# Kernel optimization log

Measured on AMD Instinct MI355X. Metric: run time of the kernel, lower is better.

Reference implementation:

```python
import jax, jax.numpy as jnp
import numpy as np

B, N, D_OBJ, D_Q, D_FUSED, D_BOX, D_ATT = 64, 36, 2048, 2048, 2048, 4, 512


def setup_inputs() -> dict:
    key = jax.random.key(0)
    ks = jax.random.split(key, 12)
    s = lambda d: 1.0 / np.sqrt(d)
    return {
        "question_embedding": jax.random.normal(ks[0], (B * N, D_Q), jnp.float32),
        "object_features_list": jax.random.normal(ks[1], (B, N, D_OBJ), jnp.float32),
        "bounding_boxes": jax.random.uniform(ks[2], (B, N, D_BOX), jnp.float32),
        "Wq": jax.random.normal(ks[3], (D_Q, D_FUSED), jnp.float32) * s(D_Q),
        "Wo": jax.random.normal(ks[4], (D_OBJ, D_FUSED), jnp.float32) * s(D_OBJ),
        "Wfa": jax.random.normal(ks[5], (D_FUSED, D_FUSED), jnp.float32) * s(D_FUSED),
        "Wfb": jax.random.normal(ks[6], (D_FUSED, D_FUSED), jnp.float32) * s(D_FUSED),
        "Wba": jax.random.normal(ks[7], (D_BOX, D_FUSED), jnp.float32) * s(D_BOX),
        "Wbb": jax.random.normal(ks[8], (D_BOX, D_FUSED), jnp.float32) * s(D_BOX),
        "W0": jax.random.normal(ks[9], (D_FUSED, D_ATT), jnp.float32) * s(D_FUSED),
        "b0": jnp.zeros((D_ATT,), jnp.float32),
        "W1": jax.random.normal(ks[10], (D_ATT, 1), jnp.float32) * s(D_ATT),
        "b1": jnp.zeros((1,), jnp.float32),
        "batch_size": B,
        "num_obj": N,
    }


def reference(question_embedding, object_features_list, bounding_boxes,
              Wq, Wo, Wfa, Wfb, Wba, Wbb, W0, b0, W1, b1,
              batch_size, num_obj):
    # fuse_object_features_with_questions: MLB fusion of question and objects
    obj_flat = object_features_list.reshape(batch_size * num_obj, -1)  # [BN, D]
    fused = (question_embedding @ Wq) * (obj_flat @ Wo)                # [BN, Df]
    fused = fused.reshape(batch_size, num_obj, -1)                     # [B, N, Df]

    # pairwise: project once, broadcast-multiply instead of materializing
    # expanded [B*N*N, D] operands (same math as expand+view+fusion).
    ra = fused @ Wfa                 # [B, N, Df]
    rb = fused @ Wfb                 # [B, N, Df]
    ba = bounding_boxes @ Wba        # [B, N, Df]
    bb = bounding_boxes @ Wbb        # [B, N, Df]
    # relations[b, i, j, :] = fusion_fused(f_i, f_j) + fusion_box(box_i, box_j)
    relations = ra[:, :, None, :] * rb[:, None, :, :] + ba[:, :, None, :] * bb[:, None, :, :]  # [B,N,N,Df]

    # compute_relation_attention: linear-tanh-linear, softmax over dim=2
    h = jnp.tanh(relations @ W0 + b0)          # [B, N, N, D_att]
    scores = h @ W1 + b1                       # [B, N, N, 1]
    att = jax.nn.softmax(scores, axis=2)[..., 0]  # [B, N, N]
    e_hat = jnp.sum(relations * att[..., None], axis=2)  # [B, N, Df]

    pairwise_res = fused + e_hat
    return object_features_list + pairwise_res
```

## Files before the change

### kernel.cpp

```cpp
#include <hip/hip_runtime.h>
#include <hip/hip_bf16.h>
#include <math.h>

constexpr int kB    = 64;
constexpr int kN    = 36;
constexpr int kBN   = kB * kN;
constexpr int kD    = 2048;
constexpr int kDatt = 512;
constexpr int kPairs = kN * kN;

using bf16x8 = __attribute__((ext_vector_type(8))) short;
using f32x4  = __attribute__((ext_vector_type(4))) float;

typedef unsigned int u32;
typedef __attribute__((address_space(3))) u32 lds_u32;
typedef const __attribute__((address_space(1))) u32 glb_u32;

__device__ inline unsigned short f2bf(float f) {
    union { float f; unsigned u; } v; v.f = f;
    unsigned r = v.u + 0x7FFFu + ((v.u >> 16) & 1u);
    return (unsigned short)(r >> 16);
}

__global__ __launch_bounds__(256)
void kcvt(const float* __restrict__ x, unsigned short* __restrict__ y, int n4)
{
    int i = blockIdx.x * 256 + threadIdx.x;
    if (i < n4) {
        float4 v = ((const float4*)x)[i];
        ushort4 o = {f2bf(v.x), f2bf(v.y), f2bf(v.z), f2bf(v.w)};
        ((ushort4*)y)[i] = o;
    }
}

__global__ __launch_bounds__(256)
void ktrp(const float* __restrict__ W, unsigned short* __restrict__ WT, int nt)
{
    __shared__ float T[64][65];
    const int k0 = blockIdx.x * 64;
    const int n0 = blockIdx.y * 64;
    const int c = threadIdx.x & 63, r0 = threadIdx.x >> 6;
    #pragma unroll
    for (int rr = 0; rr < 64; rr += 4)
        T[r0 + rr][c] = W[(size_t)(k0 + r0 + rr) * nt + n0 + c];
    __syncthreads();
    #pragma unroll
    for (int rr = 0; rr < 64; rr += 4)
        WT[(size_t)(n0 + r0 + rr) * kD + k0 + c] = f2bf(T[c][r0 + rr]);
}

__global__ __launch_bounds__(64)
void krepack_w0(const unsigned short* __restrict__ W0T, unsigned short* __restrict__ W0s)
{
    const int kb    = blockIdx.x;
    const int chunk = blockIdx.y;
    const int g     = threadIdx.x;
    const int row = chunk * 16 + (g & 7) + ((g >> 5) << 3);
    const int cg8 = ((g >> 3) & 3) * 8;
    const uint4 v = *(const uint4*)&W0T[(size_t)row * kD + kb * 32 + cg8];
    *(uint4*)&W0s[(size_t)kb * 16384 + chunk * 512 + g * 8] = v;
}

__global__ __launch_bounds__(128)
void kgbox(const float* __restrict__ Wba, const float* __restrict__ Wbb,
           const float* __restrict__ W0, float* __restrict__ G)
{
    const int uv = blockIdx.x;
    const int u = uv >> 2, v = uv & 3;
    const int c = blockIdx.y * 128 + threadIdx.x;
    float acc = 0.f;
    for (int k = 0; k < kD; k += 4) {
        #pragma unroll
        for (int t = 0; t < 4; ++t)
            acc = fmaf(Wba[u * kD + k + t] * Wbb[v * kD + k + t],
                       W0[(size_t)(k + t) * kDatt + c], acc);
    }
    G[(size_t)uv * kDatt + c] = acc;
}

__global__ __launch_bounds__(64)
void krepack_g(const float* __restrict__ G, unsigned short* __restrict__ W0s)
{
    const int chunk = blockIdx.x;
    const int g     = threadIdx.x;
    const int col = chunk * 16 + (g & 7) + ((g >> 5) << 3);
    const int kg  = (g >> 3) & 3;
    unsigned short o[8];
    #pragma unroll
    for (int e = 0; e < 8; ++e) {
        int kl = kg * 8 + e;
        o[e] = (kl < 16) ? f2bf(G[(size_t)kl * kDatt + col]) : (unsigned short)0;
    }
    *(uint4*)&W0s[(size_t)64 * 16384 + chunk * 512 + g * 8] = *(uint4*)o;
}

__global__ __launch_bounds__(256)
void k3_box_proj(const float* __restrict__ box, const float* __restrict__ Wba,
                 const float* __restrict__ Wbb,
                 float* __restrict__ ba, float* __restrict__ bb)
{
    const int r = blockIdx.y;
    const int c = blockIdx.x * 256 + threadIdx.x;
    const float x0 = box[r * 4 + 0], x1 = box[r * 4 + 1];
    const float x2 = box[r * 4 + 2], x3 = box[r * 4 + 3];
    float va = x0 * Wba[c] + x1 * Wba[kD + c] + x2 * Wba[2 * kD + c] + x3 * Wba[3 * kD + c];
    float vb = x0 * Wbb[c] + x1 * Wbb[kD + c] + x2 * Wbb[2 * kD + c] + x3 * Wbb[3 * kD + c];
    ba[(size_t)r * kD + c] = va;
    bb[(size_t)r * kD + c] = vb;
}

__device__ inline void stage128(const unsigned short* __restrict__ g,
                                int grow0, int k0,
                                unsigned short* lds, int w, int lane)
{
    const int sr = lane >> 2, sc = (lane & 3) * 8;
    #pragma unroll
    for (int t = 0; t < 2; ++t) {
        int r = w * 32 + t * 16;
        const unsigned short* gp = g + (size_t)(grow0 + r + sr) * kD + k0 + sc;
        __builtin_amdgcn_global_load_lds((glb_u32*)gp, (lds_u32*)(lds + r * 32), 16, 0, 0);
    }
}
__device__ inline void stage64(const unsigned short* __restrict__ g,
                               int grow0, int k0,
                               unsigned short* lds, int w, int lane)
{
    const int sr = lane >> 2, sc = (lane & 3) * 8;
    int r = w * 16;
    const unsigned short* gp = g + (size_t)(grow0 + r + sr) * kD + k0 + sc;
    __builtin_amdgcn_global_load_lds((glb_u32*)gp, (lds_u32*)(lds + r * 32), 16, 0, 0);
}

__global__ __launch_bounds__(256, 2)
void k1_dual_mfma(const unsigned short* __restrict__ Qb,
                  const unsigned short* __restrict__ WqT,
                  const unsigned short* __restrict__ Ob,
                  const unsigned short* __restrict__ WoT,
                  unsigned short* __restrict__ fusedb)
{
    __shared__ __align__(16) unsigned short As1[128][32];
    __shared__ __align__(16) unsigned short As2[128][32];
    __shared__ __align__(16) unsigned short Bs1[64][32];
    __shared__ __align__(16) unsigned short Bs2[64][32];

    const int tid = threadIdx.x;
    const int lane = tid & 63;
    const int w = tid >> 6;
    const int wm = w >> 1, wn = w & 1;
    const int row0 = blockIdx.y * 128;
    const int col0 = blockIdx.x * 64;

    f32x4 acc1[4][2], acc2[4][2];
    #pragma unroll
    for (int mt = 0; mt < 4; ++mt)
        #pragma unroll
        for (int nt = 0; nt < 2; ++nt) { acc1[mt][nt] = (f32x4)(0.f); acc2[mt][nt] = (f32x4)(0.f); }

    const int fr = lane & 15, ko = (lane >> 4) * 8;

    for (int k0 = 0; k0 < kD; k0 += 32) {
        stage128(Qb,  row0, k0, &As1[0][0], w, lane);
        stage128(Ob,  row0, k0, &As2[0][0], w, lane);
        stage64 (WqT, col0, k0, &Bs1[0][0], w, lane);
        stage64 (WoT, col0, k0, &Bs2[0][0], w, lane);
        __syncthreads();

        bf16x8 a1[4], a2[4];
        #pragma unroll
        for (int mt = 0; mt < 4; ++mt) {
            a1[mt] = *(bf16x8*)&As1[wm * 64 + mt * 16 + fr][ko];
            a2[mt] = *(bf16x8*)&As2[wm * 64 + mt * 16 + fr][ko];
        }
        #pragma unroll
        for (int nt = 0; nt < 2; ++nt) {
            bf16x8 b1 = *(bf16x8*)&Bs1[wn * 32 + nt * 16 + fr][ko];
            bf16x8 b2 = *(bf16x8*)&Bs2[wn * 32 + nt * 16 + fr][ko];
            #pragma unroll
            for (int mt = 0; mt < 4; ++mt) {
                acc1[mt][nt] = __builtin_amdgcn_mfma_f32_16x16x32_bf16(a1[mt], b1, acc1[mt][nt], 0, 0, 0);
                acc2[mt][nt] = __builtin_amdgcn_mfma_f32_16x16x32_bf16(a2[mt], b2, acc2[mt][nt], 0, 0, 0);
            }
        }
        __syncthreads();
    }

    const int fq = lane >> 4;
    #pragma unroll
    for (int mt = 0; mt < 4; ++mt)
        #pragma unroll
        for (int nt = 0; nt < 2; ++nt) {
            int row = row0 + wm * 64 + mt * 16 + fq * 4;
            int col = col0 + wn * 32 + nt * 16 + fr;
            #pragma unroll
            for (int reg = 0; reg < 4; ++reg) {
                float v = acc1[mt][nt][reg] * acc2[mt][nt][reg];
                fusedb[(size_t)(row + reg) * kD + col] = f2bf(v);
            }
        }
}

__global__ __launch_bounds__(256, 2)
void k2_dual_mfma(const unsigned short* __restrict__ Fb,
                  const unsigned short* __restrict__ WfaT,
                  const unsigned short* __restrict__ WfbT,
                  float* __restrict__ ra, float* __restrict__ rb)
{
    __shared__ __align__(16) unsigned short As [128][32];
    __shared__ __align__(16) unsigned short Bs1[64][32];
    __shared__ __align__(16) unsigned short Bs2[64][32];

    const int tid = threadIdx.x;
    const int lane = tid & 63;
    const int w = tid >> 6;
    const int wm = w >> 1, wn = w & 1;
    const int row0 = blockIdx.y * 128;
    const int col0 = blockIdx.x * 64;

    f32x4 acc1[4][2], acc2[4][2];
    #pragma unroll
    for (int mt = 0; mt < 4; ++mt)
        #pragma unroll
        for (int nt = 0; nt < 2; ++nt) { acc1[mt][nt] = (f32x4)(0.f); acc2[mt][nt] = (f32x4)(0.f); }

    const int fr = lane & 15, ko = (lane >> 4) * 8;

    for (int k0 = 0; k0 < kD; k0 += 32) {
        stage128(Fb,   row0, k0, &As [0][0], w, lane);
        stage64 (WfaT, col0, k0, &Bs1[0][0], w, lane);
        stage64 (WfbT, col0, k0, &Bs2[0][0], w, lane);
        __syncthreads();

        bf16x8 a[4];
        #pragma unroll
        for (int mt = 0; mt < 4; ++mt)
            a[mt] = *(bf16x8*)&As[wm * 64 + mt * 16 + fr][ko];
        #pragma unroll
        for (int nt = 0; nt < 2; ++nt) {
            bf16x8 b1 = *(bf16x8*)&Bs1[wn * 32 + nt * 16 + fr][ko];
            bf16x8 b2 = *(bf16x8*)&Bs2[wn * 32 + nt * 16 + fr][ko];
            #pragma unroll
            for (int mt = 0; mt < 4; ++mt) {
                acc1[mt][nt] = __builtin_amdgcn_mfma_f32_16x16x32_bf16(a[mt], b1, acc1[mt][nt], 0, 0, 0);
                acc2[mt][nt] = __builtin_amdgcn_mfma_f32_16x16x32_bf16(a[mt], b2, acc2[mt][nt], 0, 0, 0);
            }
        }
        __syncthreads();
    }

    const int fq = lane >> 4;
    #pragma unroll
    for (int mt = 0; mt < 4; ++mt)
        #pragma unroll
        for (int nt = 0; nt < 2; ++nt) {
            int row = row0 + wm * 64 + mt * 16 + fq * 4;
            int col = col0 + wn * 32 + nt * 16 + fr;
            #pragma unroll
            for (int reg = 0; reg < 4; ++reg) {
                size_t o = (size_t)(row + reg) * kD + col;
                ra[o] = acc1[mt][nt][reg];
                rb[o] = acc2[mt][nt][reg];
            }
        }
}

__global__ __launch_bounds__(1024)
void k4_scores_mfma(const float* __restrict__ ra, const float* __restrict__ rb,
                    const float* __restrict__ box,
                    const unsigned short* __restrict__ W0s,
                    const float* __restrict__ b0, const float* __restrict__ W1,
                    float* __restrict__ scores)
{
    __shared__ __align__(16) unsigned short Bs[2][512 * 32];
    __shared__ __align__(16) unsigned short RelS[2][128][40];
    __shared__ __align__(16) float4 Stg4[2][378];
    __shared__ float scoreS[128];

    const int tid  = threadIdx.x;
    const int lane = tid & 63;
    const int w    = tid >> 6;
    const int wm   = w >> 3;
    const int wn   = w & 7;

    const int work = (blockIdx.x & 7) * 88 + (blockIdx.x >> 3);
    const int b    = work / 11;
    const int tile = work - b * 11;
    const int p0   = tile * 128;
    const int i0   = p0 / kN;

    const float* raB  = ra  + (size_t)b * kN * kD;
    const float* rbB  = rb  + (size_t)b * kN * kD;
    const float* boxB = box + (size_t)b * kN * 4;

    const bool hasStage = (tid < 336);
    const float* sptr;
    int sdst;
    {
        int s = hasStage ? tid : 335;
        int row = s >> 3, q = s & 7;
        int grow; const float* base;
        if (row < 6) {
            int il = (row < 5) ? row : 4;
            grow = i0 + il; if (grow > kN - 1) grow = kN - 1;
            base = raB;
        } else {
            grow = row - 6;
            base = rbB;
        }
        sptr = base + (size_t)grow * kD + q * 4;
        sdst = row * 9 + q;
    }

    int rowA, cgA, ilA, iA, jA;
    {
        rowA = tid >> 3; cgA = tid & 7;
        int p = p0 + rowA; if (p >= kPairs) p = kPairs - 1;
        iA  = p / kN;
        jA  = p - iA * kN;
        ilA = iA - i0;
    }

    const int fr = lane & 15, fq = lane >> 4;
    const int bco = ((fr & 7) << 3) + ((fr >> 3) << 8) + (fq << 6);

    f32x4 acc[4][4];
    #pragma unroll
    for (int mt = 0; mt < 4; ++mt)
        #pragma unroll
        for (int nt = 0; nt < 4; ++nt)
            acc[mt][nt] = (f32x4)(0.f);

    if (tid < 128) scoreS[tid] = 0.f;

    float4 sreg0;

    #define ISSUE_B(k0_, buf_)                                                   \
        _Pragma("unroll")                                                        \
        for (int t = 0; t < 2; ++t) {                                            \
            int chunk = w * 2 + t;                                               \
            const unsigned short* gp = W0s + (size_t)((k0_) >> 5) * 16384        \
                                       + chunk * 512 + lane * 8;                 \
            __builtin_amdgcn_global_load_lds((glb_u32*)gp,                       \
                (lds_u32*)&Bs[buf_][chunk * 512], 16, 0, 0);                     \
        }

    #define STAGE_LOAD(k0_) {                                                    \
            if (hasStage) sreg0 = *(const float4*)(sptr + (k0_));                \
        }

    #define STAGE_WRITE(buf_) {                                                  \
            if (hasStage) Stg4[buf_][sdst] = sreg0;                              \
        }

    #define REL_GEN(buf_) {                                                      \
            float4 va = Stg4[buf_][ilA * 9 + cgA];                               \
            float4 vr = Stg4[buf_][(6 + jA) * 9 + cgA];                          \
            ushort4 o;                                                           \
            o.x = f2bf(va.x * vr.x);                                             \
            o.y = f2bf(va.y * vr.y);                                             \
            o.z = f2bf(va.z * vr.z);                                             \
            o.w = f2bf(va.w * vr.w);                                             \
            *(ushort4*)&RelS[buf_][rowA][cgA * 4] = o;                           \
        }

    #define REL_GEN_BOX(buf_) {                                                  \
            ushort4 o = {0, 0, 0, 0};                                            \
            if (cgA < 4) {                                                       \
                float4 bi = *(const float4*)(boxB + iA * 4);                     \
                float4 bj = *(const float4*)(boxB + jA * 4);                     \
                float biu = (cgA == 0) ? bi.x : (cgA == 1) ? bi.y                \
                          : (cgA == 2) ? bi.z : bi.w;                            \
                o.x = f2bf(biu * bj.x);                                          \
                o.y = f2bf(biu * bj.y);                                          \
                o.z = f2bf(biu * bj.z);                                          \
                o.w = f2bf(biu * bj.w);                                          \
            }                                                                    \
            *(ushort4*)&RelS[buf_][rowA][cgA * 4] = o;                           \
        }

    STAGE_LOAD(0)
    STAGE_WRITE(0)
    STAGE_LOAD(32)
    __syncthreads();
    REL_GEN(0)
    STAGE_WRITE(1)
    ISSUE_B(0, 0)

    for (int k = 0; k <= 64; ++k) {
        const int cur = k & 1, nxt = cur ^ 1;
        __syncthreads();
        if (k < 62) STAGE_LOAD((k + 2) * 32)
        if (k < 64) ISSUE_B((k + 1) * 32, nxt)
        bf16x8 af[4];
        #pragma unroll
        for (int mt = 0; mt < 4; ++mt)
            af[mt] = *(bf16x8*)&RelS[cur][wm * 64 + mt * 16 + fr][fq * 8];
        #pragma unroll
        for (int nt = 0; nt < 4; ++nt) {
            bf16x8 bfv = *(bf16x8*)&Bs[cur][wn * 2048 + nt * 512 + bco];
            #pragma unroll
            for (int mt = 0; mt < 4; ++mt)
                acc[mt][nt] = __builtin_amdgcn_mfma_f32_16x16x32_bf16(af[mt], bfv, acc[mt][nt], 0, 0, 0);
        }
        if (k < 62) STAGE_WRITE(cur)
        if (k < 63) REL_GEN(nxt)
        else if (k == 63) REL_GEN_BOX(nxt)
    }

    float b0v[4], w1v[4];
    #pragma unroll
    for (int nt = 0; nt < 4; ++nt) {
        int col = wn * 64 + nt * 16 + fr;
        b0v[nt] = b0[col];
        w1v[nt] = W1[col];
    }
    #pragma unroll
    for (int mt = 0; mt < 4; ++mt) {
        #pragma unroll
        for (int reg = 0; reg < 4; ++reg) {
            float p = 0.f;
            #pragma unroll
            for (int nt = 0; nt < 4; ++nt)
                p += w1v[nt] * tanhf(acc[mt][nt][reg] + b0v[nt]);
            p += __shfl_xor(p, 1, 64);
            p += __shfl_xor(p, 2, 64);
            p += __shfl_xor(p, 4, 64);
            p += __shfl_xor(p, 8, 64);
            if (fr == 0)
                atomicAdd(&scoreS[wm * 64 + mt * 16 + fq * 4 + reg], p);
        }
    }
    __syncthreads();
    if (tid < 128 && p0 + tid < kPairs)
        scores[(size_t)b * kPairs + p0 + tid] = scoreS[tid];
}

__global__ __launch_bounds__(64)
void k5_softmax(const float* __restrict__ scores, float* __restrict__ att)
{
    const int bi = blockIdx.x;
    const int tid = threadIdx.x;
    float s = (tid < kN) ? scores[(size_t)bi * kN + tid] : -1e30f;
    float m = s;
    #pragma unroll
    for (int off = 32; off >= 1; off >>= 1)
        m = fmaxf(m, __shfl_xor(m, off, 64));
    float e = (tid < kN) ? expf(s - m) : 0.f;
    float sum = e;
    #pragma unroll
    for (int off = 32; off >= 1; off >>= 1)
        sum += __shfl_xor(sum, off, 64);
    if (tid < kN) att[(size_t)bi * kN + tid] = e / sum;
}

__global__ __launch_bounds__(256)
void k6_output(const float* __restrict__ obj, const unsigned short* __restrict__ fusedb,
               const float* __restrict__ ra, const float* __restrict__ ba,
               const float* __restrict__ rb, const float* __restrict__ bb,
               const float* __restrict__ att, float* __restrict__ out)
{
    __shared__ float attS[kN];
    const int bi = blockIdx.x;
    const int b = bi / kN;
    const int tid = threadIdx.x;
    if (tid < kN) attS[tid] = att[(size_t)bi * kN + tid];
    __syncthreads();
    for (int d = tid; d < kD; d += 256) {
        float s1 = 0.f, s2 = 0.f;
        #pragma unroll 4
        for (int j = 0; j < kN; ++j) {
            float a = attS[j];
            size_t rrow = (size_t)(b * kN + j) * kD + d;
            s1 = fmaf(a, rb[rrow], s1);
            s2 = fmaf(a, bb[rrow], s2);
        }
        size_t o = (size_t)bi * kD + d;
        float fv = __uint_as_float((u32)fusedb[o] << 16);
        out[o] = obj[o] + fv + ra[o] * s1 + ba[o] * s2;
    }
}

extern "C" void kernel_launch(void* const* d_in, const int* in_sizes, int n_in,
                              void* d_out, int out_size, void* d_ws, size_t ws_size,
                              hipStream_t stream)
{
    const float* q   = (const float*)d_in[0];
    const float* obj = (const float*)d_in[1];
    const float* box = (const float*)d_in[2];
    const float* Wq  = (const float*)d_in[3];
    const float* Wo  = (const float*)d_in[4];
    const float* Wfa = (const float*)d_in[5];
    const float* Wfb = (const float*)d_in[6];
    const float* Wba = (const float*)d_in[7];
    const float* Wbb = (const float*)d_in[8];
    const float* W0  = (const float*)d_in[9];
    const float* b0v = (const float*)d_in[10];
    const float* W1  = (const float*)d_in[11];
    float* out = (float*)d_out;

    const size_t nBD = (size_t)kBN * kD;
    float* ws = (float*)d_ws;
    size_t off = 0;
    float* ra     = ws + off; off += nBD;
    float* rb     = ws + off; off += nBD;
    float* ba     = ws + off; off += nBD;
    float* bb     = ws + off; off += nBD;
    float* scores = ws + off; off += (size_t)kBN * kN;
    float* att    = ws + off; off += (size_t)kBN * kN;
    float* G      = ws + off; off += (size_t)16 * kDatt;

    unsigned short* us = (unsigned short*)(ws + off);
    size_t uoff = 0;
    unsigned short* W0T     = us + uoff; uoff += (size_t)kDatt * kD;
    unsigned short* W0s     = us + uoff; uoff += (size_t)65 * 16384;
    unsigned short* q_bf    = us + uoff; uoff += nBD;
    unsigned short* obj_bf  = us + uoff; uoff += nBD;
    unsigned short* fusedbf = us + uoff; uoff += nBD;
    unsigned short* WqT     = us + uoff; uoff += (size_t)kD * kD;
    unsigned short* WoT     = us + uoff; uoff += (size_t)kD * kD;
    unsigned short* WfaT = q_bf;
    unsigned short* WfbT = obj_bf;

    const int n4 = (int)(nBD / 4);
    kcvt<<<dim3((n4 + 255) / 256), 256, 0, stream>>>(q,   q_bf,   n4);
    kcvt<<<dim3((n4 + 255) / 256), 256, 0, stream>>>(obj, obj_bf, n4);
    ktrp<<<dim3(32, 32), 256, 0, stream>>>(Wq, WqT, kD);
    ktrp<<<dim3(32, 32), 256, 0, stream>>>(Wo, WoT, kD);
    ktrp<<<dim3(32, 8),  256, 0, stream>>>(W0, W0T, kDatt);
    krepack_w0<<<dim3(kD / 32, kDatt / 16), 64, 0, stream>>>(W0T, W0s);
    kgbox<<<dim3(16, 4), 128, 0, stream>>>(Wba, Wbb, W0, G);
    krepack_g<<<dim3(32), 64, 0, stream>>>(G, W0s);
    k3_box_proj<<<dim3(kD / 256, kBN), 256, 0, stream>>>(box, Wba, Wbb, ba, bb);

    k1_dual_mfma<<<dim3(kD / 64, kBN / 128), 256, 0, stream>>>(q_bf, WqT, obj_bf, WoT, fusedbf);

    ktrp<<<dim3(32, 32), 256, 0, stream>>>(Wfa, WfaT, kD);
    ktrp<<<dim3(32, 32), 256, 0, stream>>>(Wfb, WfbT, kD);

    k2_dual_mfma<<<dim3(kD / 64, kBN / 128), 256, 0, stream>>>(fusedbf, WfaT, WfbT, ra, rb);

    k4_scores_mfma<<<dim3(kB * 11), 1024, 0, stream>>>(ra, rb, box, W0s, b0v, W1, scores);
    k5_softmax<<<kBN, 64, 0, stream>>>(scores, att);
    k6_output<<<kBN, 256, 0, stream>>>(obj, fusedbf, ra, ba, rb, bb, att, out);
}
```

Measured before the change: 760.9 us.

## Eliminate ba/bb materialization via attention-weighted boxes and split-K kgbox

Removes the k3_box_proj kernel and the two full [BN,2048] fp32 ba/bb buffers. The softmax kernel now also computes the attention-weighted box sum per row, and the output kernel rebuilds ba and the weighted bb sum on the fly from the 4-wide box projections, so bb is never streamed per j. kgbox is also restructured as a split-K kernel computing all 16 box-pair products per thread, with partial sums reduced in krepack_g, to use more parallelism than the old 64-block grid. This saves large memory writes and reads at the cost of a few extra FMAs and small weight loads in the output kernel.

```diff
diff --git a/kernel.cpp b/kernel.cpp
--- a/kernel.cpp
+++ b/kernel.cpp
@@ -61,25 +61,51 @@
     *(uint4*)&W0s[(size_t)kb * 16384 + chunk * 512 + g * 8] = v;
 }
 
-__global__ __launch_bounds__(128)
+__global__ __launch_bounds__(256)
 void kgbox(const float* __restrict__ Wba, const float* __restrict__ Wbb,
-           const float* __restrict__ W0, float* __restrict__ G)
-{
-    const int uv = blockIdx.x;
-    const int u = uv >> 2, v = uv & 3;
-    const int c = blockIdx.y * 128 + threadIdx.x;
-    float acc = 0.f;
-    for (int k = 0; k < kD; k += 4) {
-        #pragma unroll
-        for (int t = 0; t < 4; ++t)
-            acc = fmaf(Wba[u * kD + k + t] * Wbb[v * kD + k + t],
-                       W0[(size_t)(k + t) * kDatt + c], acc);
-    }
-    G[(size_t)uv * kDatt + c] = acc;
+           const float* __restrict__ W0, float* __restrict__ Gpart)
+{
+    __shared__ float red[4][64][17];
+    const int ct = blockIdx.x;
+    const int kc = blockIdx.y;
+    const int cl = threadIdx.x & 63;
+    const int kq = threadIdx.x >> 6;
+    const int c  = ct * 64 + cl;
+
+    float acc[16];
+    #pragma unroll
+    for (int t = 0; t < 16; ++t) acc[t] = 0.f;
+
+    const int kbase = kc * 128 + kq * 32;
+    for (int kk = 0; kk < 32; ++kk) {
+        int k = kbase + kk;
+        float w0 = W0[(size_t)k * kDatt + c];
+        float a0 = Wba[k], a1 = Wba[kD + k], a2 = Wba[2 * kD + k], a3 = Wba[3 * kD + k];
+        float b0 = Wbb[k] * w0, b1 = Wbb[kD + k] * w0,
+              b2 = Wbb[2 * kD + k] * w0, b3 = Wbb[3 * kD + k] * w0;
+        acc[0]  = fmaf(a0, b0, acc[0]);  acc[1]  = fmaf(a0, b1, acc[1]);
+        acc[2]  = fmaf(a0, b2, acc[2]);  acc[3]  = fmaf(a0, b3, acc[3]);
+        acc[4]  = fmaf(a1, b0, acc[4]);  acc[5]  = fmaf(a1, b1, acc[5]);
+        acc[6]  = fmaf(a1, b2, acc[6]);  acc[7]  = fmaf(a1, b3, acc[7]);
+        acc[8]  = fmaf(a2, b0, acc[8]);  acc[9]  = fmaf(a2, b1, acc[9]);
+        acc[10] = fmaf(a2, b2, acc[10]); acc[11] = fmaf(a2, b3, acc[11]);
+        acc[12] = fmaf(a3, b0, acc[12]); acc[13] = fmaf(a3, b1, acc[13]);
+        acc[14] = fmaf(a3, b2, acc[14]); acc[15] = fmaf(a3, b3, acc[15]);
+    }
+    #pragma unroll
+    for (int t = 0; t < 16; ++t) red[kq][cl][t] = acc[t];
+    __syncthreads();
+    #pragma unroll
+    for (int t = 0; t < 4; ++t) {
+        int s = threadIdx.x + t * 256;
+        int cc = s >> 4, uv = s & 15;
+        float v = red[0][cc][uv] + red[1][cc][uv] + red[2][cc][uv] + red[3][cc][uv];
+        Gpart[((size_t)kc * 16 + uv) * kDatt + ct * 64 + cc] = v;
+    }
 }
 
 __global__ __launch_bounds__(64)
-void krepack_g(const float* __restrict__ G, unsigned short* __restrict__ W0s)
+void krepack_g(const float* __restrict__ Gpart, unsigned short* __restrict__ W0s)
 {
     const int chunk = blockIdx.x;
     const int g     = threadIdx.x;
@@ -89,24 +115,15 @@
     #pragma unroll
     for (int e = 0; e < 8; ++e) {
         int kl = kg * 8 + e;
-        o[e] = (kl < 16) ? f2bf(G[(size_t)kl * kDatt + col]) : (unsigned short)0;
+        if (kl < 16) {
+            float s = 0.f;
+            #pragma unroll
+            for (int kc = 0; kc < 16; ++kc)
+                s += Gpart[((size_t)kc * 16 + kl) * kDatt + col];
+            o[e] = f2bf(s);
+        } else o[e] = 0;
     }
     *(uint4*)&W0s[(size_t)64 * 16384 + chunk * 512 + g * 8] = *(uint4*)o;
-}
-
-__global__ __launch_bounds__(256)
-void k3_box_proj(const float* __restrict__ box, const float* __restrict__ Wba,
-                 const float* __restrict__ Wbb,
-                 float* __restrict__ ba, float* __restrict__ bb)
-{
-    const int r = blockIdx.y;
-    const int c = blockIdx.x * 256 + threadIdx.x;
-    const float x0 = box[r * 4 + 0], x1 = box[r * 4 + 1];
-    const float x2 = box[r * 4 + 2], x3 = box[r * 4 + 3];
-    float va = x0 * Wba[c] + x1 * Wba[kD + c] + x2 * Wba[2 * kD + c] + x3 * Wba[3 * kD + c];
-    float vb = x0 * Wbb[c] + x1 * Wbb[kD + c] + x2 * Wbb[2 * kD + c] + x3 * Wbb[3 * kD + c];
-    ba[(size_t)r * kD + c] = va;
-    bb[(size_t)r * kD + c] = vb;
 }
 
 __device__ inline void stage128(const unsigned short* __restrict__ g,
@@ -435,9 +452,11 @@
 }
 
 __global__ __launch_bounds__(64)
-void k5_softmax(const float* __restrict__ scores, float* __restrict__ att)
+void k5_softmax(const float* __restrict__ scores, const float* __restrict__ box,
+                float* __restrict__ att, float* __restrict__ abox)
 {
     const int bi = blockIdx.x;
+    const int b  = bi / kN;
     const int tid = threadIdx.x;
     float s = (tid < kN) ? scores[(size_t)bi * kN + tid] : -1e30f;
     float m = s;
@@ -449,14 +468,29 @@
     #pragma unroll
     for (int off = 32; off >= 1; off >>= 1)
         sum += __shfl_xor(sum, off, 64);
-    if (tid < kN) att[(size_t)bi * kN + tid] = e / sum;
+    float a = e / sum;
+    if (tid < kN) att[(size_t)bi * kN + tid] = a;
+
+    float4 bx = {0.f, 0.f, 0.f, 0.f};
+    if (tid < kN) bx = *(const float4*)(box + (size_t)(b * kN + tid) * 4);
+    bx.x *= a; bx.y *= a; bx.z *= a; bx.w *= a;
+    #pragma unroll
+    for (int off = 32; off >= 1; off >>= 1) {
+        bx.x += __shfl_xor(bx.x, off, 64);
+        bx.y += __shfl_xor(bx.y, off, 64);
+        bx.z += __shfl_xor(bx.z, off, 64);
+        bx.w += __shfl_xor(bx.w, off, 64);
+    }
+    if (tid == 0) *(float4*)(abox + (size_t)bi * 4) = bx;
 }
 
 __global__ __launch_bounds__(256)
 void k6_output(const float* __restrict__ obj, const unsigned short* __restrict__ fusedb,
-               const float* __restrict__ ra, const float* __restrict__ ba,
-               const float* __restrict__ rb, const float* __restrict__ bb,
-               const float* __restrict__ att, float* __restrict__ out)
+               const float* __restrict__ ra, const float* __restrict__ rb,
+               const float* __restrict__ att, const float* __restrict__ box,
+               const float* __restrict__ abox,
+               const float* __restrict__ Wba, const float* __restrict__ Wbb,
+               float* __restrict__ out)
 {
     __shared__ float attS[kN];
     const int bi = blockIdx.x;
@@ -464,18 +498,20 @@
     const int tid = threadIdx.x;
     if (tid < kN) attS[tid] = att[(size_t)bi * kN + tid];
     __syncthreads();
+    const float4 bxi = *(const float4*)(box  + (size_t)bi * 4);
+    const float4 axi = *(const float4*)(abox + (size_t)bi * 4);
     for (int d = tid; d < kD; d += 256) {
-        float s1 = 0.f, s2 = 0.f;
+        float s1 = 0.f;
         #pragma unroll 4
-        for (int j = 0; j < kN; ++j) {
-            float a = attS[j];
-            size_t rrow = (size_t)(b * kN + j) * kD + d;
-            s1 = fmaf(a, rb[rrow], s1);
-            s2 = fmaf(a, bb[rrow], s2);
-        }
+        for (int j = 0; j < kN; ++j)
+            s1 = fmaf(attS[j], rb[(size_t)(b * kN + j) * kD + d], s1);
+        float bav = bxi.x * Wba[d] + bxi.y * Wba[kD + d]
+                  + bxi.z * Wba[2 * kD + d] + bxi.w * Wba[3 * kD + d];
+        float s2  = axi.x * Wbb[d] + axi.y * Wbb[kD + d]
+                  + axi.z * Wbb[2 * kD + d] + axi.w * Wbb[3 * kD + d];
         size_t o = (size_t)bi * kD + d;
         float fv = __uint_as_float((u32)fusedb[o] << 16);
-        out[o] = obj[o] + fv + ra[o] * s1 + ba[o] * s2;
+        out[o] = obj[o] + fv + ra[o] * s1 + bav * s2;
     }
 }
 
@@ -502,11 +538,10 @@
     size_t off = 0;
     float* ra     = ws + off; off += nBD;
     float* rb     = ws + off; off += nBD;
-    float* ba     = ws + off; off += nBD;
-    float* bb     = ws + off; off += nBD;
     float* scores = ws + off; off += (size_t)kBN * kN;
     float* att    = ws + off; off += (size_t)kBN * kN;
-    float* G      = ws + off; off += (size_t)16 * kDatt;
+    float* abox   = ws + off; off += (size_t)kBN * 4;
+    float* Gpart  = ws + off; off += (size_t)16 * 16 * kDatt;
 
     unsigned short* us = (unsigned short*)(ws + off);
     size_t uoff = 0;
@@ -527,9 +562,8 @@
     ktrp<<<dim3(32, 32), 256, 0, stream>>>(Wo, WoT, kD);
     ktrp<<<dim3(32, 8),  256, 0, stream>>>(W0, W0T, kDatt);
     krepack_w0<<<dim3(kD / 32, kDatt / 16), 64, 0, stream>>>(W0T, W0s);
-    kgbox<<<dim3(16, 4), 128, 0, stream>>>(Wba, Wbb, W0, G);
-    krepack_g<<<dim3(32), 64, 0, stream>>>(G, W0s);
-    k3_box_proj<<<dim3(kD / 256, kBN), 256, 0, stream>>>(box, Wba, Wbb, ba, bb);
+    kgbox<<<dim3(8, 16), 256, 0, stream>>>(Wba, Wbb, W0, Gpart);
+    krepack_g<<<dim3(32), 64, 0, stream>>>(Gpart, W0s);
 
     k1_dual_mfma<<<dim3(kD / 64, kBN / 128), 256, 0, stream>>>(q_bf, WqT, obj_bf, WoT, fusedbf);
 
@@ -539,6 +573,6 @@
     k2_dual_mfma<<<dim3(kD / 64, kBN / 128), 256, 0, stream>>>(fusedbf, WfaT, WfbT, ra, rb);
 
     k4_scores_mfma<<<dim3(kB * 11), 1024, 0, stream>>>(ra, rb, box, W0s, b0v, W1, scores);
-    k5_softmax<<<kBN, 64, 0, stream>>>(scores, att);
-    k6_output<<<kBN, 256, 0, stream>>>(obj, fusedbf, ra, ba, rb, bb, att, out);
-}
+    k5_softmax<<<kBN, 64, 0, stream>>>(scores, box, att, abox);
+    k6_output<<<kBN, 256, 0, stream>>>(obj, fusedbf, ra, rb, att, box, abox, Wba, Wbb, out);
+}
```

Result: faster. 646.6 us (-15.0%).
